# Optimization experiments

Measured on AMD Instinct MI355X. Metric: run time of the kernel, lower is better.

Reference implementation:

```python
import jax, jax.numpy as jnp
import numpy as np


def _feature_map(x):
    # elu(x) + 1, the canonical positive feature map for linear attention
    return jax.nn.elu(x) + 1.0


def setup_inputs() -> dict:
    key = jax.random.key(0)
    kq, kk, kv = jax.random.split(key, 3)
    B, T, H, D, M = 2, 2048, 8, 64, 64
    q = jax.random.normal(kq, (B, T, H, D), dtype=jnp.float32)
    k = jax.random.normal(kk, (B, T, H, D), dtype=jnp.float32)
    v = jax.random.normal(kv, (B, T, H, M), dtype=jnp.float32)
    return {"q": q, "k": k, "v": v}


def reference(q, k, v):
    # q,k: [B,T,H,D]; v: [B,T,H,M]
    qf = _feature_map(q)
    kf = _feature_map(k)
    # running sum of keys over time (causal)
    k_sum = jnp.cumsum(kf, axis=1)                      # [B,T,H,D]
    z = 1.0 / jnp.einsum('bthd,bthd->bth', qf, k_sum)   # [B,T,H]
    # outer products k_i v_i^T; NOTE: original torch code cumsums over dim=-2
    # (the D axis of the [B,T,H,D,M] tensor), reproduced faithfully here.
    kv = jnp.einsum('bthd,bthm->bthdm', kf, v)           # [B,T,H,D,M]
    kv_sum = jnp.cumsum(kv, axis=-2)                     # cumsum over D, per source
    out = jnp.einsum('bthd,bthdm,bth->bthm', qf, kv_sum, z)
    return out
```

## Files before the change

### kernel.cpp

```cpp
#include <hip/hip_runtime.h>
#include <hip/hip_bf16.h>

#define BB 2
#define TT 2048
#define HH 8
#define DD 64
#define CC 256
#define TC (TT / CC)
#define STRIDE (HH * DD)
#define NBH (BB * HH)
#define PW (CC / 16)

__device__ __forceinline__ float feat(float x) {
    return x > 0.f ? x + 1.f : __expf(x);
}

__global__ void __launch_bounds__(64)
chunk_sums_kernel(const float* __restrict__ k, float* __restrict__ ws) {
    const int idx  = blockIdx.x;
    const int c    = idx & (CC - 1);
    const int h    = (idx >> 8) & (HH - 1);
    const int b    = idx >> 11;
    const int lane = threadIdx.x;

    size_t base = (((size_t)b * TT + c * TC) * HH + h) * DD + lane;

    float kv[TC];
    #pragma unroll
    for (int i = 0; i < TC; ++i) kv[i] = k[base + (size_t)i * STRIDE];

    float s = 0.f;
    #pragma unroll
    for (int i = 0; i < TC; ++i) s += feat(kv[i]);
    ws[(size_t)idx * DD + lane] = s;
}

__global__ void __launch_bounds__(1024)
prefix_kernel(float* __restrict__ ws) {
    const int bh   = blockIdx.x;
    const int lane = threadIdx.x & 63;
    const int w    = threadIdx.x >> 6;

    size_t base = ((size_t)bh * CC + w * PW) * DD + lane;

    float val[PW];
    #pragma unroll
    for (int i = 0; i < PW; ++i) val[i] = ws[base + (size_t)i * DD];

    float run = 0.f, excl[PW];
    #pragma unroll
    for (int i = 0; i < PW; ++i) { excl[i] = run; run += val[i]; }

    __shared__ float tot[16][DD];
    tot[w][lane] = run;
    __syncthreads();

    float carry = 0.f;
    for (int w2 = 0; w2 < w; ++w2) carry += tot[w2][lane];

    #pragma unroll
    for (int i = 0; i < PW; ++i) ws[base + (size_t)i * DD] = excl[i] + carry;
}

__global__ void __launch_bounds__(64)
linattn_kernel(const float* __restrict__ q, const float* __restrict__ k,
               const float* __restrict__ v, const float* __restrict__ ws,
               float* __restrict__ out) {
    const int idx  = blockIdx.x;
    const int c    = idx & (CC - 1);
    const int h    = (idx >> 8) & (HH - 1);
    const int b    = idx >> 11;
    const int lane = threadIdx.x;

    size_t base = (((size_t)b * TT + c * TC) * HH + h) * DD + lane;

    float kf[TC], qf[TC], vv[TC];
    #pragma unroll
    for (int i = 0; i < TC; ++i) kf[i] = k[base + (size_t)i * STRIDE];
    #pragma unroll
    for (int i = 0; i < TC; ++i) qf[i] = q[base + (size_t)i * STRIDE];
    #pragma unroll
    for (int i = 0; i < TC; ++i) vv[i] = v[base + (size_t)i * STRIDE];

    const float carry = ws[(size_t)idx * DD + lane];

    #pragma unroll
    for (int i = 0; i < TC; ++i) { kf[i] = feat(kf[i]); qf[i] = feat(qf[i]); }

    float run[TC];
    run[0] = carry + kf[0];
    #pragma unroll
    for (int i = 1; i < TC; ++i) run[i] = run[i - 1] + kf[i];

    #pragma unroll
    for (int o = 1; o < 64; o <<= 1) {
        float u[TC];
        #pragma unroll
        for (int i = 0; i < TC; ++i) u[i] = __shfl_up(kf[i], o, 64);
        #pragma unroll
        for (int i = 0; i < TC; ++i) if (lane >= o) kf[i] += u[i];
    }

    float a[TC], s[TC];
    #pragma unroll
    for (int i = 0; i < TC; ++i) { a[i] = qf[i] * run[i]; s[i] = qf[i] * kf[i]; }
    #pragma unroll
    for (int o = 32; o >= 1; o >>= 1) {
        #pragma unroll
        for (int i = 0; i < TC; ++i) {
            a[i] += __shfl_xor(a[i], o, 64);
            s[i] += __shfl_xor(s[i], o, 64);
        }
    }

    #pragma unroll
    for (int i = 0; i < TC; ++i)
        out[base + (size_t)i * STRIDE] = vv[i] * (s[i] / a[i]);
}

extern "C" void kernel_launch(void* const* d_in, const int* in_sizes, int n_in,
                              void* d_out, int out_size, void* d_ws, size_t ws_size,
                              hipStream_t stream) {
    const float* q = (const float*)d_in[0];
    const float* k = (const float*)d_in[1];
    const float* v = (const float*)d_in[2];
    float* out = (float*)d_out;
    float* ws  = (float*)d_ws;

    const int nblk = BB * HH * CC;
    chunk_sums_kernel<<<nblk, 64, 0, stream>>>(k, ws);
    prefix_kernel<<<NBH, 1024, 0, stream>>>(ws);
    linattn_kernel<<<nblk, 64, 0, stream>>>(q, k, v, ws, out);
}
```

Before: 83.23 us.

## Remap lanes to float4 across timesteps with segmented scans in chunk kernels

Both the chunk-sum and main kernels now give each lane four consecutive D elements (float4) for two timesteps, so 16 lanes cover D and 4 lane groups cover timesteps. Loads and stores become 128-bit vector accesses. The time-axis cumsum and the D-axis scan and reduction are redone with width-16 shuffles plus in-register prefix sums, which cuts the shuffle count sharply compared with scanning each of 8 rows across 64 lanes. The trade-off is more intricate index and scan logic, with the same memory traffic.

```diff
diff --git a/kernel.cpp b/kernel.cpp
--- a/kernel.cpp
+++ b/kernel.cpp
@@ -15,6 +15,7 @@
     return x > 0.f ? x + 1.f : __expf(x);
 }
 
+
 __global__ void __launch_bounds__(64)
 chunk_sums_kernel(const float* __restrict__ k, float* __restrict__ ws) {
     const int idx  = blockIdx.x;
@@ -22,17 +23,26 @@
     const int h    = (idx >> 8) & (HH - 1);
     const int b    = idx >> 11;
     const int lane = threadIdx.x;
+    const int g    = lane & 15;
+    const int seg  = lane >> 4;
 
-    size_t base = (((size_t)b * TT + c * TC) * HH + h) * DD + lane;
+    const size_t off0 = (((size_t)b * TT + c * TC + seg) * HH + h) * DD + g * 4;
+    const float4 k0 = *(const float4*)(k + off0);
+    const float4 k1 = *(const float4*)(k + off0 + (size_t)4 * STRIDE);
 
-    float kv[TC];
-    #pragma unroll
-    for (int i = 0; i < TC; ++i) kv[i] = k[base + (size_t)i * STRIDE];
+    float4 s;
+    s.x = feat(k0.x) + feat(k1.x);
+    s.y = feat(k0.y) + feat(k1.y);
+    s.z = feat(k0.z) + feat(k1.z);
+    s.w = feat(k0.w) + feat(k1.w);
 
-    float s = 0.f;
-    #pragma unroll
-    for (int i = 0; i < TC; ++i) s += feat(kv[i]);
-    ws[(size_t)idx * DD + lane] = s;
+    s.x += __shfl_xor(s.x, 16, 64); s.y += __shfl_xor(s.y, 16, 64);
+    s.z += __shfl_xor(s.z, 16, 64); s.w += __shfl_xor(s.w, 16, 64);
+    s.x += __shfl_xor(s.x, 32, 64); s.y += __shfl_xor(s.y, 32, 64);
+    s.z += __shfl_xor(s.z, 32, 64); s.w += __shfl_xor(s.w, 32, 64);
+
+    if (seg == 0)
+        *(float4*)(ws + (size_t)idx * DD + g * 4) = s;
 }
 
 __global__ void __launch_bounds__(1024)
@@ -71,51 +81,92 @@
     const int h    = (idx >> 8) & (HH - 1);
     const int b    = idx >> 11;
     const int lane = threadIdx.x;
+    const int g    = lane & 15;
+    const int seg  = lane >> 4;
 
-    size_t base = (((size_t)b * TT + c * TC) * HH + h) * DD + lane;
+    const size_t off0 = (((size_t)b * TT + c * TC + seg) * HH + h) * DD + g * 4;
+    const size_t off1 = off0 + (size_t)4 * STRIDE;
 
-    float kf[TC], qf[TC], vv[TC];
+    float4 kf0 = *(const float4*)(k + off0);
+    float4 kf1 = *(const float4*)(k + off1);
+    float4 qf0 = *(const float4*)(q + off0);
+    float4 qf1 = *(const float4*)(q + off1);
+    const float4 vv0 = *(const float4*)(v + off0);
+    const float4 vv1 = *(const float4*)(v + off1);
+    const float4 carry = *(const float4*)(ws + (size_t)idx * DD + g * 4);
+
+    kf0.x = feat(kf0.x); kf0.y = feat(kf0.y); kf0.z = feat(kf0.z); kf0.w = feat(kf0.w);
+    kf1.x = feat(kf1.x); kf1.y = feat(kf1.y); kf1.z = feat(kf1.z); kf1.w = feat(kf1.w);
+    qf0.x = feat(qf0.x); qf0.y = feat(qf0.y); qf0.z = feat(qf0.z); qf0.w = feat(qf0.w);
+    qf1.x = feat(qf1.x); qf1.y = feat(qf1.y); qf1.z = feat(qf1.z); qf1.w = feat(qf1.w);
+
+    float4 i0 = kf0, i1 = kf1;
+    {
+        float u;
+        u = __shfl_up(i0.x, 16, 64); if (seg >= 1) i0.x += u;
+        u = __shfl_up(i0.y, 16, 64); if (seg >= 1) i0.y += u;
+        u = __shfl_up(i0.z, 16, 64); if (seg >= 1) i0.z += u;
+        u = __shfl_up(i0.w, 16, 64); if (seg >= 1) i0.w += u;
+        u = __shfl_up(i1.x, 16, 64); if (seg >= 1) i1.x += u;
+        u = __shfl_up(i1.y, 16, 64); if (seg >= 1) i1.y += u;
+        u = __shfl_up(i1.z, 16, 64); if (seg >= 1) i1.z += u;
+        u = __shfl_up(i1.w, 16, 64); if (seg >= 1) i1.w += u;
+        u = __shfl_up(i0.x, 32, 64); if (seg >= 2) i0.x += u;
+        u = __shfl_up(i0.y, 32, 64); if (seg >= 2) i0.y += u;
+        u = __shfl_up(i0.z, 32, 64); if (seg >= 2) i0.z += u;
+        u = __shfl_up(i0.w, 32, 64); if (seg >= 2) i0.w += u;
+        u = __shfl_up(i1.x, 32, 64); if (seg >= 2) i1.x += u;
+        u = __shfl_up(i1.y, 32, 64); if (seg >= 2) i1.y += u;
+        u = __shfl_up(i1.z, 32, 64); if (seg >= 2) i1.z += u;
+        u = __shfl_up(i1.w, 32, 64); if (seg >= 2) i1.w += u;
+    }
+    float4 S0;
+    S0.x = __shfl(i0.x, 48 + g, 64);
+    S0.y = __shfl(i0.y, 48 + g, 64);
+    S0.z = __shfl(i0.z, 48 + g, 64);
+    S0.w = __shfl(i0.w, 48 + g, 64);
+
+    float4 run0, run1;
+    run0.x = carry.x + i0.x; run0.y = carry.y + i0.y;
+    run0.z = carry.z + i0.z; run0.w = carry.w + i0.w;
+    run1.x = carry.x + S0.x + i1.x; run1.y = carry.y + S0.y + i1.y;
+    run1.z = carry.z + S0.z + i1.z; run1.w = carry.w + S0.w + i1.w;
+
+    float4 p0, p1;
+    p0.x = kf0.x; p0.y = p0.x + kf0.y; p0.z = p0.y + kf0.z; p0.w = p0.z + kf0.w;
+    p1.x = kf1.x; p1.y = p1.x + kf1.y; p1.z = p1.y + kf1.z; p1.w = p1.z + kf1.w;
+    float c0 = p0.w, c1 = p1.w;
     #pragma unroll
-    for (int i = 0; i < TC; ++i) kf[i] = k[base + (size_t)i * STRIDE];
+    for (int o = 1; o <= 8; o <<= 1) {
+        float u0 = __shfl_up(c0, o, 16);
+        float u1 = __shfl_up(c1, o, 16);
+        if (g >= o) { c0 += u0; c1 += u1; }
+    }
+    const float e0 = c0 - p0.w;
+    const float e1 = c1 - p1.w;
+    float4 pre0, pre1;
+    pre0.x = p0.x + e0; pre0.y = p0.y + e0; pre0.z = p0.z + e0; pre0.w = p0.w + e0;
+    pre1.x = p1.x + e1; pre1.y = p1.y + e1; pre1.z = p1.z + e1; pre1.w = p1.w + e1;
+
+    float s1_0 = qf0.x * pre0.x + qf0.y * pre0.y + qf0.z * pre0.z + qf0.w * pre0.w;
+    float s2_0 = qf0.x * run0.x + qf0.y * run0.y + qf0.z * run0.z + qf0.w * run0.w;
+    float s1_1 = qf1.x * pre1.x + qf1.y * pre1.y + qf1.z * pre1.z + qf1.w * pre1.w;
+    float s2_1 = qf1.x * run1.x + qf1.y * run1.y + qf1.z * run1.z + qf1.w * run1.w;
     #pragma unroll
-    for (int i = 0; i < TC; ++i) qf[i] = q[base + (size_t)i * STRIDE];
-    #pragma unroll
-    for (int i = 0; i < TC; ++i) vv[i] = v[base + (size_t)i * STRIDE];
-
-    const float carry = ws[(size_t)idx * DD + lane];
-
-    #pragma unroll
-    for (int i = 0; i < TC; ++i) { kf[i] = feat(kf[i]); qf[i] = feat(qf[i]); }
-
-    float run[TC];
-    run[0] = carry + kf[0];
-    #pragma unroll
-    for (int i = 1; i < TC; ++i) run[i] = run[i - 1] + kf[i];
-
-    #pragma unroll
-    for (int o = 1; o < 64; o <<= 1) {
-        float u[TC];
-        #pragma unroll
-        for (int i = 0; i < TC; ++i) u[i] = __shfl_up(kf[i], o, 64);
-        #pragma unroll
-        for (int i = 0; i < TC; ++i) if (lane >= o) kf[i] += u[i];
+    for (int o = 1; o <= 8; o <<= 1) {
+        s1_0 += __shfl_xor(s1_0, o, 64);
+        s2_0 += __shfl_xor(s2_0, o, 64);
+        s1_1 += __shfl_xor(s1_1, o, 64);
+        s2_1 += __shfl_xor(s2_1, o, 64);
     }
 
-    float a[TC], s[TC];
-    #pragma unroll
-    for (int i = 0; i < TC; ++i) { a[i] = qf[i] * run[i]; s[i] = qf[i] * kf[i]; }
-    #pragma unroll
-    for (int o = 32; o >= 1; o >>= 1) {
-        #pragma unroll
-        for (int i = 0; i < TC; ++i) {
-            a[i] += __shfl_xor(a[i], o, 64);
-            s[i] += __shfl_xor(s[i], o, 64);
-        }
-    }
-
-    #pragma unroll
-    for (int i = 0; i < TC; ++i)
-        out[base + (size_t)i * STRIDE] = vv[i] * (s[i] / a[i]);
+    const float r0 = s1_0 / s2_0;
+    const float r1 = s1_1 / s2_1;
+    float4 o0, o1;
+    o0.x = vv0.x * r0; o0.y = vv0.y * r0; o0.z = vv0.z * r0; o0.w = vv0.w * r0;
+    o1.x = vv1.x * r1; o1.y = vv1.y * r1; o1.z = vv1.z * r1; o1.w = vv1.w * r1;
+    *(float4*)(out + off0) = o0;
+    *(float4*)(out + off1) = o1;
 }
 
 extern "C" void kernel_launch(void* const* d_in, const int* in_sizes, int n_in,
```

Result: faster. 80.34 us (-3.5%).
